# Kernel optimization log

Hardware: AMD Instinct MI355X
Metric: run time of the kernel (lower is better)

Reference implementation:

```python
import jax, jax.numpy as jnp
import numpy as np

N_BOX = 1000000


def box2corners(box):
    # box: (N,5) = x,y,w,h,alpha -> corners (N,4,2), order matches lilanxiao/Rotated_IoU
    x, y, w, h, a = (box[:, i] for i in range(5))
    dx = jnp.array([0.5, -0.5, -0.5, 0.5], box.dtype)
    dy = jnp.array([0.5, 0.5, -0.5, -0.5], box.dtype)
    cx = dx[None, :] * w[:, None]
    cy = dy[None, :] * h[:, None]
    c, s = jnp.cos(a)[:, None], jnp.sin(a)[:, None]
    rx = cx * c - cy * s + x[:, None]
    ry = cx * s + cy * c + y[:, None]
    return jnp.stack([rx, ry], axis=-1)


def edge_intersections(c1, c2):
    # all 4x4 edge-pair intersections; strict interior criterion (0<t<1, 0<u<1)
    p1, p2 = c1, jnp.roll(c1, -1, axis=1)
    p3, p4 = c2, jnp.roll(c2, -1, axis=1)
    x1, y1 = p1[:, :, None, 0], p1[:, :, None, 1]
    x2, y2 = p2[:, :, None, 0], p2[:, :, None, 1]
    x3, y3 = p3[:, None, :, 0], p3[:, None, :, 1]
    x4, y4 = p4[:, None, :, 0], p4[:, None, :, 1]
    num_t = (x2 - x1) * (y3 - y1) - (y2 - y1) * (x3 - x1)
    den_t = (x2 - x1) * (y3 - y4) - (y2 - y1) * (x3 - x4)
    t = jnp.where(den_t == 0., -1., num_t / jnp.where(den_t == 0., 1., den_t))
    mask_t = (t > 0.) & (t < 1.)
    num_u = (x4 - x3) * (y1 - y3) - (y4 - y3) * (x1 - x3)
    den_u = (x4 - x3) * (y1 - y2) - (y4 - y3) * (x1 - x2)
    u = jnp.where(den_u == 0., -1., num_u / jnp.where(den_u == 0., 1., den_u))
    mask = mask_t & (u > 0.) & (u < 1.)
    tx = x1 + t * (x2 - x1)
    ty = y1 + t * (y2 - y1)
    pts = jnp.stack([tx, ty], axis=-1) * mask[..., None]
    n = c1.shape[0]
    return pts.reshape(n, 16, 2), mask.reshape(n, 16)


def box_in_box(corners1, corners2):
    # projection test: is each corner of box1 inside rectangle box2
    a = corners2[:, 0:1, :]
    b = corners2[:, 1:2, :]
    d = corners2[:, 3:4, :]
    ab, ad, am = b - a, d - a, corners1 - a
    p_ab = (ab * am).sum(-1) / (ab * ab).sum(-1)
    p_ad = (ad * am).sum(-1) / (ad * ad).sum(-1)
    eps = 1e-6
    return (p_ab > -eps) & (p_ab < 1. + eps) & (p_ad > -eps) & (p_ad < 1. + eps)


def intersection_area(c1, c2):
    # convex intersection polygon: 24 candidate vertices, sort valid ones by angle, shoelace
    pts, m_int = edge_intersections(c1, c2)
    m1 = box_in_box(c1, c2)
    m2 = box_in_box(c2, c1)
    verts = jnp.concatenate([c1, c2, pts], axis=1)   # (N,24,2)
    mask = jnp.concatenate([m1, m2, m_int], axis=1)  # (N,24)
    k = mask.sum(axis=1)
    mean = (verts * mask[..., None]).sum(1, keepdims=True) / jnp.maximum(k, 1)[:, None, None]
    v = jnp.where(mask[..., None], verts - mean, 0.)
    ang = jnp.where(mask, jnp.arctan2(v[..., 1], v[..., 0]), 1e9)
    order = jnp.argsort(ang, axis=1)
    vs = jnp.take_along_axis(v, order[..., None], axis=1)
    pad = jnp.arange(24)[None, :, None] < k[:, None, None]
    vs = jnp.where(pad, vs, vs[:, 0:1, :])  # pad by repeating first valid vertex -> zero cross terms
    vn = jnp.roll(vs, -1, axis=1)
    cross = vs[..., 0] * vn[..., 1] - vs[..., 1] * vn[..., 0]
    return 0.5 * jnp.abs(cross.sum(axis=1))


def riou_loss(pred, target):
    # RIOUloss(reduction='none', loss_type='iou') -> cal_diou per-box loss, loss[0]
    rad_p = jnp.arctan2(pred[:, 4], pred[:, 5])
    rad_t = jnp.arctan2(target[:, 4], target[:, 5])
    b1 = jnp.concatenate([pred[:, :4], rad_p[:, None]], axis=1)
    b2 = jnp.concatenate([target[:, :4], rad_t[:, None]], axis=1)
    c1 = box2corners(b1)
    c2 = box2corners(b2)
    inter = intersection_area(c1, c2)
    area1 = b1[:, 2] * b1[:, 3]
    area2 = b2[:, 2] * b2[:, 3]
    union = area1 + area2 - inter
    iou = inter / union
    allc = jnp.concatenate([c1, c2], axis=1)  # (N,8,2) enclosing box (axis-aligned)
    wc = allc[..., 0].max(1) - allc[..., 0].min(1)
    hc = allc[..., 1].max(1) - allc[..., 1].min(1)
    c2diag = wc * wc + hc * hc
    d2 = (b1[:, 0] - b2[:, 0]) ** 2 + (b1[:, 1] - b2[:, 1]) ** 2
    return 1. - iou + d2 / c2diag


def setup_inputs() -> dict:
    key = jax.random.key(0)
    k1, k2, k3, k4 = jax.random.split(key, 4)
    n = N_BOX
    xy = jax.random.uniform(k1, (n, 2)) * 640.
    wh = jax.random.uniform(k2, (n, 2)) * 48. + 2.
    sc = jax.random.normal(k3, (n, 2)) + 0.1
    pred = jnp.concatenate([xy, wh, sc], axis=1)
    k5, k6, k7 = jax.random.split(k4, 3)
    t_xy = xy + jax.random.normal(k5, (n, 2)) * 8.
    t_wh = jnp.abs(wh * (1. + 0.2 * jax.random.normal(k6, (n, 2)))) + 1.
    t_sc = sc + 0.3 * jax.random.normal(k7, (n, 2))
    target = jnp.concatenate([t_xy, t_wh, t_sc], axis=1)
    return {"pred": pred, "target": target}


def reference(pred, target):
    return riou_loss(pred, target)
```

## Files before the change

kernel.cpp:

```cpp
#include <hip/hip_runtime.h>
#include <math.h>


#define FMUL __fmul_rn
#define FADD __fadd_rn
#define FSUB __fsub_rn
#define FDIV __fdiv_rn

__device__ __forceinline__ float rcpf_(float x) { return __builtin_amdgcn_rcpf(x); }

__global__ __launch_bounds__(256, 2)
void riou_kernel(const float* __restrict__ pred,
                 const float* __restrict__ tgt,
                 float* __restrict__ out, int n)
{
    int i = blockIdx.x * blockDim.x + threadIdx.x;
    if (i >= n) return;

    const float* p = pred + 6 * (size_t)i;
    const float* q = tgt  + 6 * (size_t)i;

    const float px = p[0], py = p[1], pw = p[2], ph = p[3];
    const float qx = q[0], qy = q[1], qw = q[2], qh = q[3];

    float rad1 = atan2f(p[4], p[5]);
    float cA = cosf(rad1), sA = sinf(rad1);
    float rad2 = atan2f(q[4], q[5]);
    float cB = cosf(rad2), sB = sinf(rad2);

    const float ddx[4] = {0.5f, -0.5f, -0.5f, 0.5f};
    const float ddy[4] = {0.5f, 0.5f, -0.5f, -0.5f};
    float c1x[4], c1y[4], c2x[4], c2y[4];
#pragma unroll
    for (int j = 0; j < 4; j++) {
        float cx = FMUL(ddx[j], pw), cy = FMUL(ddy[j], ph);
        c1x[j] = FADD(FSUB(FMUL(cx, cA), FMUL(cy, sA)), px);
        c1y[j] = FADD(FADD(FMUL(cx, sA), FMUL(cy, cA)), py);
        float dx2 = FMUL(ddx[j], qw), dy2 = FMUL(ddy[j], qh);
        c2x[j] = FADD(FSUB(FMUL(dx2, cB), FMUL(dy2, sB)), qx);
        c2y[j] = FADD(FADD(FMUL(dx2, sB), FMUL(dy2, cB)), qy);
    }

    float minx = c1x[0], maxx = c1x[0], miny = c1y[0], maxy = c1y[0];
#pragma unroll
    for (int j = 1; j < 4; j++) {
        minx = fminf(minx, c1x[j]); maxx = fmaxf(maxx, c1x[j]);
        miny = fminf(miny, c1y[j]); maxy = fmaxf(maxy, c1y[j]);
    }
#pragma unroll
    for (int j = 0; j < 4; j++) {
        minx = fminf(minx, c2x[j]); maxx = fmaxf(maxx, c2x[j]);
        miny = fminf(miny, c2y[j]); maxy = fmaxf(maxy, c2y[j]);
    }
    float wcb = FSUB(maxx, minx), hcb = FSUB(maxy, miny);
    float c2d = FADD(FMUL(wcb, wcb), FMUL(hcb, hcb));
    float dxc = FSUB(px, qx), dyc = FSUB(py, qy);
    float d2 = FADD(FMUL(dxc, dxc), FMUL(dyc, dyc));

    float vx[24], vy[24];
    unsigned mbits = 0;
    int k = 0;
    float sx = 0.0f, sy = 0.0f;
    const float eps = 1e-6f;
    const float hieps = 1.0f + 1e-6f;

    {
        float ax = c2x[0], ay = c2y[0];
        float abx = FSUB(c2x[1], ax), aby = FSUB(c2y[1], ay);
        float adx = FSUB(c2x[3], ax), ady = FSUB(c2y[3], ay);
        float rab = rcpf_(FADD(FMUL(abx, abx), FMUL(aby, aby)));
        float rad = rcpf_(FADD(FMUL(adx, adx), FMUL(ady, ady)));
#pragma unroll
        for (int j = 0; j < 4; j++) {
            float amx = FSUB(c1x[j], ax), amy = FSUB(c1y[j], ay);
            float pab = FMUL(FADD(FMUL(abx, amx), FMUL(aby, amy)), rab);
            float pad = FMUL(FADD(FMUL(adx, amx), FMUL(ady, amy)), rad);
            int m = (pab > -eps) & (pab < hieps) & (pad > -eps) & (pad < hieps);
            vx[j] = c1x[j]; vy[j] = c1y[j];
            mbits |= (unsigned)m << j;
            k += m;
            sx = FADD(sx, m ? c1x[j] : 0.0f);
            sy = FADD(sy, m ? c1y[j] : 0.0f);
        }
    }
    {
        float ax = c1x[0], ay = c1y[0];
        float abx = FSUB(c1x[1], ax), aby = FSUB(c1y[1], ay);
        float adx = FSUB(c1x[3], ax), ady = FSUB(c1y[3], ay);
        float rab = rcpf_(FADD(FMUL(abx, abx), FMUL(aby, aby)));
        float rad = rcpf_(FADD(FMUL(adx, adx), FMUL(ady, ady)));
#pragma unroll
        for (int j = 0; j < 4; j++) {
            float amx = FSUB(c2x[j], ax), amy = FSUB(c2y[j], ay);
            float pab = FMUL(FADD(FMUL(abx, amx), FMUL(aby, amy)), rab);
            float pad = FMUL(FADD(FMUL(adx, amx), FMUL(ady, amy)), rad);
            int m = (pab > -eps) & (pab < hieps) & (pad > -eps) & (pad < hieps);
            vx[4 + j] = c2x[j]; vy[4 + j] = c2y[j];
            mbits |= (unsigned)m << (4 + j);
            k += m;
            sx = FADD(sx, m ? c2x[j] : 0.0f);
            sy = FADD(sy, m ? c2y[j] : 0.0f);
        }
    }
    float fex[4], fey[4];
#pragma unroll
    for (int e2 = 0; e2 < 4; e2++) {
        fex[e2] = FSUB(c2x[(e2 + 1) & 3], c2x[e2]);
        fey[e2] = FSUB(c2y[(e2 + 1) & 3], c2y[e2]);
    }
#pragma unroll
    for (int e1 = 0; e1 < 4; e1++) {
        float x1 = c1x[e1], y1 = c1y[e1];
        float ex = FSUB(c1x[(e1 + 1) & 3], x1), ey = FSUB(c1y[(e1 + 1) & 3], y1);
#pragma unroll
        for (int e2 = 0; e2 < 4; e2++) {
            float dx31 = FSUB(c2x[e2], x1), dy31 = FSUB(c2y[e2], y1);
            float num_t = FSUB(FMUL(ex, dy31), FMUL(ey, dx31));
            float den_t = FSUB(FMUL(ey, fex[e2]), FMUL(ex, fey[e2]));
            float rd = rcpf_(den_t);
            float tq = FMUL(num_t, rd);
            float num_u = FSUB(FMUL(fey[e2], dx31), FMUL(fex[e2], dy31));
            float uq = FMUL(num_u, rd);
            int m = (tq > 0.0f) & (tq < 1.0f) & (uq < 0.0f) & (uq > -1.0f);
            float ix = FADD(x1, FMUL(tq, ex));
            float iy = FADD(y1, FMUL(tq, ey));
            int s = 8 + 4 * e1 + e2;
            vx[s] = ix; vy[s] = iy;
            mbits |= (unsigned)m << s;
            k += m;
            sx = FADD(sx, m ? ix : 0.0f);
            sy = FADD(sy, m ? iy : 0.0f);
        }
    }

    float kk = (float)(k > 0 ? k : 1);
    float mx = FDIV(sx, kk), my = FDIV(sy, kk);

    unsigned pk[24];
#pragma unroll
    for (int j = 0; j < 24; j++) {
        int m = (mbits >> j) & 1u;
        float wx2 = m ? FSUB(vx[j], mx) : 0.0f;
        float wy2 = m ? FSUB(vy[j], my) : 0.0f;
        vx[j] = wx2; vy[j] = wy2;
        float dsum = FADD(fabsf(wx2), fabsf(wy2));
        float rs = (dsum > 0.0f) ? FMUL(wx2, rcpf_(dsum)) : 1.0f;
        float keyf = copysignf(FSUB(1.0f, rs), wy2);
        unsigned sb = __float_as_uint(keyf);
        unsigned u = sb ^ (unsigned)(((int)sb >> 31) | (int)0x80000000);
        pk[j] = m ? ((u & 0xFFFFFFE0u) | (unsigned)j)
                  : (0xFFFFFFE0u | (unsigned)j);
    }

    const unsigned MASKED_MIN = 0xFFFFFFE0u;
    unsigned prevkey = 0;
    float firstx, firsty, prevx, prevy;
    float crs = 0.0f;
    {
        unsigned best = MASKED_MIN; float bx = 0.0f, by = 0.0f;
#pragma unroll
        for (int j = 0; j < 24; j++) {
            bool c = (pk[j] > prevkey) & (pk[j] < best);
            best = c ? pk[j] : best;
            bx = c ? vx[j] : bx;
            by = c ? vy[j] : by;
        }
        firstx = bx; firsty = by; prevx = bx; prevy = by; prevkey = best;
    }
#pragma unroll
    for (int s = 1; s < 8; s++) {
        unsigned best = MASKED_MIN; float bx = prevx, by = prevy;
#pragma unroll
        for (int j = 0; j < 24; j++) {
            bool c = (pk[j] > prevkey) & (pk[j] < best);
            best = c ? pk[j] : best;
            bx = c ? vx[j] : bx;
            by = c ? vy[j] : by;
        }
        crs = FADD(crs, FSUB(FMUL(prevx, by), FMUL(prevy, bx)));
        prevx = bx; prevy = by; prevkey = best;
    }
    for (int s = 8; s < k; s++) {
        unsigned best = MASKED_MIN; float bx = prevx, by = prevy;
#pragma unroll
        for (int j = 0; j < 24; j++) {
            bool c = (pk[j] > prevkey) & (pk[j] < best);
            best = c ? pk[j] : best;
            bx = c ? vx[j] : bx;
            by = c ? vy[j] : by;
        }
        crs = FADD(crs, FSUB(FMUL(prevx, by), FMUL(prevy, bx)));
        prevx = bx; prevy = by; prevkey = best;
    }
    crs = FADD(crs, FSUB(FMUL(prevx, firsty), FMUL(prevy, firstx)));
    float inter = FMUL(0.5f, fabsf(crs));

    float area1 = FMUL(pw, ph), area2 = FMUL(qw, qh);
    float uni = FSUB(FADD(area1, area2), inter);
    float iou = FMUL(inter, rcpf_(uni));

    out[i] = FADD(FSUB(1.0f, iou), FMUL(d2, rcpf_(c2d)));
}

extern "C" void kernel_launch(void* const* d_in, const int* in_sizes, int n_in,
                              void* d_out, int out_size, void* d_ws, size_t ws_size,
                              hipStream_t stream) {
    const float* pred = (const float*)d_in[0];
    const float* tgt  = (const float*)d_in[1];
    float* out = (float*)d_out;
    int n = in_sizes[0] / 6;
    int block = 256;
    int grid = (n + block - 1) / block;
    riou_kernel<<<grid, block, 0, stream>>>(pred, tgt, out, n);
}
```

Baseline: 131.3 us.

## Restructure selection-sort polygon ordering with offset-unsigned compare and tree reduction

```diff
diff --git a/kernel.cpp b/kernel.cpp
--- a/kernel.cpp
+++ b/kernel.cpp
@@ -17,15 +17,16 @@
     int i = blockIdx.x * blockDim.x + threadIdx.x;
     if (i >= n) return;
 
-    const float* p = pred + 6 * (size_t)i;
-    const float* q = tgt  + 6 * (size_t)i;
-
-    const float px = p[0], py = p[1], pw = p[2], ph = p[3];
-    const float qx = q[0], qy = q[1], qw = q[2], qh = q[3];
-
-    float rad1 = atan2f(p[4], p[5]);
+    const float2* p2 = (const float2*)(pred + 6 * (size_t)i);
+    const float2* q2 = (const float2*)(tgt  + 6 * (size_t)i);
+    float2 pa = p2[0], pb = p2[1], pc2 = p2[2];
+    float2 qa = q2[0], qb = q2[1], qc2 = q2[2];
+    const float px = pa.x, py = pa.y, pw = pb.x, ph = pb.y;
+    const float qx = qa.x, qy = qa.y, qw = qb.x, qh = qb.y;
+
+    float rad1 = atan2f(pc2.x, pc2.y);
     float cA = cosf(rad1), sA = sinf(rad1);
-    float rad2 = atan2f(q[4], q[5]);
+    float rad2 = atan2f(qc2.x, qc2.y);
     float cB = cosf(rad2), sB = sinf(rad2);
 
     const float ddx[4] = {0.5f, -0.5f, -0.5f, 0.5f};
@@ -59,7 +60,6 @@
 
     float vx[24], vy[24];
     unsigned mbits = 0;
-    int k = 0;
     float sx = 0.0f, sy = 0.0f;
     const float eps = 1e-6f;
     const float hieps = 1.0f + 1e-6f;
@@ -78,7 +78,6 @@
             int m = (pab > -eps) & (pab < hieps) & (pad > -eps) & (pad < hieps);
             vx[j] = c1x[j]; vy[j] = c1y[j];
             mbits |= (unsigned)m << j;
-            k += m;
             sx = FADD(sx, m ? c1x[j] : 0.0f);
             sy = FADD(sy, m ? c1y[j] : 0.0f);
         }
@@ -97,7 +96,6 @@
             int m = (pab > -eps) & (pab < hieps) & (pad > -eps) & (pad < hieps);
             vx[4 + j] = c2x[j]; vy[4 + j] = c2y[j];
             mbits |= (unsigned)m << (4 + j);
-            k += m;
             sx = FADD(sx, m ? c2x[j] : 0.0f);
             sy = FADD(sy, m ? c2y[j] : 0.0f);
         }
@@ -127,12 +125,13 @@
             int s = 8 + 4 * e1 + e2;
             vx[s] = ix; vy[s] = iy;
             mbits |= (unsigned)m << s;
-            k += m;
             sx = FADD(sx, m ? ix : 0.0f);
             sy = FADD(sy, m ? iy : 0.0f);
         }
     }
 
+    int k = __popc(mbits);
+
     float kk = (float)(k > 0 ? k : 1);
     float mx = FDIV(sx, kk), my = FDIV(sy, kk);
 
@@ -140,8 +139,8 @@
 #pragma unroll
     for (int j = 0; j < 24; j++) {
         int m = (mbits >> j) & 1u;
-        float wx2 = m ? FSUB(vx[j], mx) : 0.0f;
-        float wy2 = m ? FSUB(vy[j], my) : 0.0f;
+        float wx2 = FSUB(vx[j], mx);
+        float wy2 = FSUB(vy[j], my);
         vx[j] = wx2; vy[j] = wy2;
         float dsum = FADD(fabsf(wx2), fabsf(wy2));
         float rs = (dsum > 0.0f) ? FMUL(wx2, rcpf_(dsum)) : 1.0f;
@@ -152,45 +151,65 @@
                   : (0xFFFFFFE0u | (unsigned)j);
     }
 
-    const unsigned MASKED_MIN = 0xFFFFFFE0u;
-    unsigned prevkey = 0;
-    float firstx, firsty, prevx, prevy;
+    unsigned prevkey = 0xFFFFFFFFu;
+    float firstx = 0.0f, firsty = 0.0f, prevx = 0.0f, prevy = 0.0f;
     float crs = 0.0f;
-    {
-        unsigned best = MASKED_MIN; float bx = 0.0f, by = 0.0f;
-#pragma unroll
-        for (int j = 0; j < 24; j++) {
-            bool c = (pk[j] > prevkey) & (pk[j] < best);
-            best = c ? pk[j] : best;
-            bx = c ? vx[j] : bx;
-            by = c ? vy[j] : by;
-        }
-        firstx = bx; firsty = by; prevx = bx; prevy = by; prevkey = best;
-    }
-#pragma unroll
-    for (int s = 1; s < 8; s++) {
-        unsigned best = MASKED_MIN; float bx = prevx, by = prevy;
-#pragma unroll
-        for (int j = 0; j < 24; j++) {
-            bool c = (pk[j] > prevkey) & (pk[j] < best);
-            best = c ? pk[j] : best;
-            bx = c ? vx[j] : bx;
-            by = c ? vy[j] : by;
+#pragma unroll
+    for (int s = 0; s < 8; s++) {
+        unsigned poff = prevkey + 1u;
+        unsigned cb0, cb1, cb2, cb3;
+        float cxx0, cxx1, cxx2, cxx3, cyy0, cyy1, cyy2, cyy3;
+#pragma unroll
+        for (int c = 0; c < 4; c++) {
+            unsigned b = pk[6 * c] - poff;
+            float bx = vx[6 * c], by = vy[6 * c];
+#pragma unroll
+            for (int t = 1; t < 6; t++) {
+                int j = 6 * c + t;
+                unsigned wj = pk[j] - poff;
+                bool lt = wj < b;
+                b  = lt ? wj : b;
+                bx = lt ? vx[j] : bx;
+                by = lt ? vy[j] : by;
+            }
+            if (c == 0) { cb0 = b; cxx0 = bx; cyy0 = by; }
+            else if (c == 1) { cb1 = b; cxx1 = bx; cyy1 = by; }
+            else if (c == 2) { cb2 = b; cxx2 = bx; cyy2 = by; }
+            else { cb3 = b; cxx3 = bx; cyy3 = by; }
+        }
+        bool l01 = cb1 < cb0;
+        unsigned b01 = l01 ? cb1 : cb0;
+        float x01 = l01 ? cxx1 : cxx0, y01 = l01 ? cyy1 : cyy0;
+        bool l23 = cb3 < cb2;
+        unsigned b23 = l23 ? cb3 : cb2;
+        float x23 = l23 ? cxx3 : cxx2, y23 = l23 ? cyy3 : cyy2;
+        bool lf = b23 < b01;
+        unsigned bw = lf ? b23 : b01;
+        float bx = lf ? x23 : x01, by = lf ? y23 : y01;
+        unsigned bestkey = bw + poff;
+        bool act = s < k;
+        bx = act ? bx : prevx;
+        by = act ? by : prevy;
+        if (s == 0) { firstx = bx; firsty = by; }
+        else {
+            crs = FADD(crs, FSUB(FMUL(prevx, by), FMUL(prevy, bx)));
+        }
+        prevx = bx; prevy = by; prevkey = bestkey;
+    }
+    for (int s = 8; s < k; s++) {
+        unsigned poff = prevkey + 1u;
+        unsigned best = pk[0] - poff;
+        float bx = vx[0], by = vy[0];
+#pragma unroll
+        for (int j = 1; j < 24; j++) {
+            unsigned wj = pk[j] - poff;
+            bool lt = wj < best;
+            best = lt ? wj : best;
+            bx = lt ? vx[j] : bx;
+            by = lt ? vy[j] : by;
         }
         crs = FADD(crs, FSUB(FMUL(prevx, by), FMUL(prevy, bx)));
-        prevx = bx; prevy = by; prevkey = best;
-    }
-    for (int s = 8; s < k; s++) {
-        unsigned best = MASKED_MIN; float bx = prevx, by = prevy;
-#pragma unroll
-        for (int j = 0; j < 24; j++) {
-            bool c = (pk[j] > prevkey) & (pk[j] < best);
-            best = c ? pk[j] : best;
-            bx = c ? vx[j] : bx;
-            by = c ? vy[j] : by;
-        }
-        crs = FADD(crs, FSUB(FMUL(prevx, by), FMUL(prevy, bx)));
-        prevx = bx; prevy = by; prevkey = best;
+        prevx = bx; prevy = by; prevkey = best + poff;
     }
     crs = FADD(crs, FSUB(FMUL(prevx, firsty), FMUL(prevy, firstx)));
     float inter = FMUL(0.5f, fabsf(crs));
```

Result: faster. 127.3 us (-3.0%).
